# Kernel optimization log

Hardware: AMD Instinct MI355X
Metric: run time of the kernel (lower is better)

Reference implementation:

```python
import jax, jax.numpy as jnp
import numpy as np
import math

B, T, E, H = 2, 2048, 1024, 16
HD = E // H


def layernorm(x, g, b, eps=1e-5):
    mu = jnp.mean(x, axis=-1, keepdims=True)
    var = jnp.var(x, axis=-1, keepdims=True)
    return (x - mu) * jax.lax.rsqrt(var + eps) * g + b


def new_gelu(x):
    c = math.sqrt(2.0 / math.pi)
    return 0.5 * x * (1.0 + jnp.tanh(c * (x + 0.044715 * x ** 3)))


def setup_inputs() -> dict:
    key = jax.random.key(0)
    ks = jax.random.split(key, 6)
    s = 0.02
    return {
        "x": jax.random.normal(ks[0], (B, T, E), jnp.float32),
        "ln1_g": jnp.ones((E,), jnp.float32),
        "ln1_b": jnp.zeros((E,), jnp.float32),
        "w_attn": jax.random.normal(ks[1], (E, 3 * E), jnp.float32) * s,
        "b_attn": jnp.zeros((3 * E,), jnp.float32),
        "w_proj": jax.random.normal(ks[2], (E, E), jnp.float32) * s,
        "b_proj": jnp.zeros((E,), jnp.float32),
        "ln2_g": jnp.ones((E,), jnp.float32),
        "ln2_b": jnp.zeros((E,), jnp.float32),
        "w_fc": jax.random.normal(ks[3], (E, 4 * E), jnp.float32) * s,
        "b_fc": jnp.zeros((4 * E,), jnp.float32),
        "w_fc2": jax.random.normal(ks[4], (4 * E, E), jnp.float32) * s,
        "b_fc2": jnp.zeros((E,), jnp.float32),
    }


def reference(x, ln1_g, ln1_b, w_attn, b_attn, w_proj, b_proj,
              ln2_g, ln2_b, w_fc, b_fc, w_fc2, b_fc2):
    # --- attention branch (pre-norm) ---
    h = layernorm(x, ln1_g, ln1_b)
    qkv = h @ w_attn + b_attn                      # [B,T,3E]
    q, k, v = jnp.split(qkv, 3, axis=-1)
    # [B,T,E] -> [B,H,T,HD]
    q = q.reshape(B, T, H, HD).transpose(0, 2, 1, 3)
    k = k.reshape(B, T, H, HD).transpose(0, 2, 1, 3)
    v = v.reshape(B, T, H, HD).transpose(0, 2, 1, 3)
    att = jnp.einsum('bhqd,bhkd->bhqk', q, k) * (1.0 / math.sqrt(HD))
    causal = jnp.tril(jnp.ones((T, T), bool))       # [T,T]
    att = jnp.where(causal, att, -jnp.inf)
    att = jax.nn.softmax(att, axis=-1)
    y = jnp.einsum('bhqk,bhkd->bhqd', att, v)       # [B,H,T,HD]
    y = y.transpose(0, 2, 1, 3).reshape(B, T, E)
    y = y @ w_proj + b_proj
    x = x + y
    # --- MLP branch (pre-norm) ---
    h = layernorm(x, ln2_g, ln2_b)
    h = new_gelu(h @ w_fc + b_fc)
    h = h @ w_fc2 + b_fc2
    return x + h
```

## Files before the change

### kernel.cpp

```cpp
#include <hip/hip_runtime.h>

typedef unsigned short u16;
typedef unsigned int   u32;
typedef short bf16x8 __attribute__((ext_vector_type(8)));
typedef float f32x4  __attribute__((ext_vector_type(4)));

__device__ __forceinline__ float bf_lo(u32 u){ return __uint_as_float(u << 16); }
__device__ __forceinline__ float bf_hi(u32 u){ return __uint_as_float(u & 0xffff0000u); }
__device__ __forceinline__ u16 bf16r(float f){
  u32 u = __float_as_uint(f);
  u += 0x7fffu + ((u >> 16) & 1u);
  return (u16)(u >> 16);
}
__device__ __forceinline__ u32 pack2(float a, float b){
  return (u32)bf16r(a) | ((u32)bf16r(b) << 16);
}
__device__ __forceinline__ u32 pk_trunc(float a, float b){
  return (__float_as_uint(a) >> 16) | (__float_as_uint(b) & 0xffff0000u);
}
__device__ __forceinline__ float gelu_f(float x){
  float t = 0.7978845608028654f * (x + 0.044715f * x * x * x);
  t = fminf(fmaxf(t, -12.f), 12.f);
  float e = __expf(2.f * t);
  float th = (e - 1.f) / (e + 1.f);
  return 0.5f * x * (1.f + th);
}
__device__ __forceinline__ void glds16(const void* g, void* l) {
  __builtin_amdgcn_global_load_lds(
      (const __attribute__((address_space(1))) void*)g,
      (__attribute__((address_space(3))) void*)l, 16, 0, 0);
}

#define QSCALE 0.1803368801111204f

__global__ __launch_bounds__(256) void wt_k(const float* __restrict__ W,
                                            u16* __restrict__ Wt, int K, int N) {
  __shared__ float t[32][33];
  int k0 = blockIdx.x * 32, n0 = blockIdx.y * 32;
  int tx = threadIdx.x & 31, ty = threadIdx.x >> 5;
  #pragma unroll
  for (int i = 0; i < 32; i += 8)
    t[ty + i][tx] = W[(size_t)(k0 + ty + i) * N + n0 + tx];
  __syncthreads();
  #pragma unroll
  for (int i = 0; i < 32; i += 8)
    Wt[(size_t)(n0 + ty + i) * K + k0 + tx] = bf16r(t[tx][ty + i]);
}

__global__ __launch_bounds__(256) void vt_k(const u16* __restrict__ qkv,
                                            u16* __restrict__ Vt) {
  __shared__ u16 tl[32][33];
  int t0 = blockIdx.x * 32;
  int bh = blockIdx.y >> 1, d0 = (blockIdx.y & 1) * 32;
  int bb = bh >> 4, h = bh & 15;
  int tx = threadIdx.x & 31, ty = threadIdx.x >> 5;
  #pragma unroll
  for (int i = 0; i < 32; i += 8)
    tl[ty + i][tx] = qkv[(size_t)(bb*2048 + t0 + ty + i)*3072 + 2048 + h*64 + d0 + tx];
  __syncthreads();
  #pragma unroll
  for (int i = 0; i < 32; i += 8)
    Vt[((size_t)bh*64 + d0 + ty + i)*2048 + t0 + tx] = tl[tx][ty + i];
}

__global__ __launch_bounds__(256) void ln_k(const float* __restrict__ x,
                                            const float* __restrict__ g,
                                            const float* __restrict__ bta,
                                            u16* __restrict__ out) {
  int row = blockIdx.x, tid = threadIdx.x;
  const float4 xv = ((const float4*)(x + (size_t)row * 1024))[tid];
  float s = xv.x + xv.y + xv.z + xv.w;
  float q = xv.x*xv.x + xv.y*xv.y + xv.z*xv.z + xv.w*xv.w;
  #pragma unroll
  for (int off = 32; off > 0; off >>= 1) {
    s += __shfl_down(s, off);
    q += __shfl_down(q, off);
  }
  __shared__ float ss[4], sq[4];
  if ((tid & 63) == 0) { ss[tid >> 6] = s; sq[tid >> 6] = q; }
  __syncthreads();
  s = ss[0] + ss[1] + ss[2] + ss[3];
  q = sq[0] + sq[1] + sq[2] + sq[3];
  float mu = s * (1.f/1024.f);
  float rs = rsqrtf(q * (1.f/1024.f) - mu*mu + 1e-5f);
  const float4 gv = ((const float4*)g)[tid];
  const float4 bv = ((const float4*)bta)[tid];
  uint2 o;
  o.x = pack2((xv.x-mu)*rs*gv.x + bv.x, (xv.y-mu)*rs*gv.y + bv.y);
  o.y = pack2((xv.z-mu)*rs*gv.z + bv.z, (xv.w-mu)*rs*gv.w + bv.w);
  ((uint2*)(out + (size_t)row * 1024))[tid] = o;
}

template<int MODE, int MI, int LB>
__global__ __launch_bounds__(256, LB) void gemm_k(
    const u16* __restrict__ A, const u16* __restrict__ Bt,
    const float* __restrict__ bias, const float* __restrict__ resid,
    void* __restrict__ out, int M, int N, int K, int lda)
{
  constexpr int TM = MI * 32;
  __shared__ u16 Al[TM * 64];
  __shared__ u16 Bl[128 * 64];
  const int tid = threadIdx.x;
  const int by = blockIdx.y;
  const int sp = (MODE == 5) ? (by >> 3) : 0;
  const int n0 = (MODE == 5) ? ((by & 7) * 128) : (by * 128);
  const size_t koff = (size_t)sp * K;
  const int m0 = blockIdx.x * TM;
  const int wave = tid >> 6, lane = tid & 63;
  const int wm = (wave >> 1) * (MI * 16), wn = (wave & 1) * 64;
  const int l15 = lane & 15, quad = lane >> 4;
  const int sr = lane >> 3, cs = lane & 7;
  f32x4 acc[MI][4];
  const f32x4 zero = {0.f, 0.f, 0.f, 0.f};
  #pragma unroll
  for (int i = 0; i < MI; ++i)
    #pragma unroll
    for (int j = 0; j < 4; ++j)
      acc[i][j] = zero;
  for (int k0 = 0; k0 < K; k0 += 64) {
    __syncthreads();
    #pragma unroll
    for (int it = 0; it < MI; ++it) {
      int r = it*32 + wave*8 + sr;
      int c = cs ^ (r & 7);
      glds16(&A[(size_t)(m0 + r) * lda + koff + k0 + c*8], &Al[(it*32 + wave*8) * 64]);
    }
    #pragma unroll
    for (int it = 0; it < 4; ++it) {
      int r = it*32 + wave*8 + sr;
      int c = cs ^ (r & 7);
      glds16(&Bt[(size_t)(n0 + r) * lda + koff + k0 + c*8], &Bl[(it*32 + wave*8) * 64]);
    }
    __syncthreads();
    #pragma unroll
    for (int kk = 0; kk < 2; ++kk) {
      bf16x8 af[MI], bfr[4];
      #pragma unroll
      for (int i = 0; i < MI; ++i) {
        int R = wm + i*16 + l15;
        af[i] = *(const bf16x8*)&Al[R*64 + ((kk*4 + quad) ^ (R & 7)) * 8];
      }
      #pragma unroll
      for (int j = 0; j < 4; ++j) {
        int R = wn + j*16 + l15;
        bfr[j] = *(const bf16x8*)&Bl[R*64 + ((kk*4 + quad) ^ (R & 7)) * 8];
      }
      #pragma unroll
      for (int i = 0; i < MI; ++i)
        #pragma unroll
        for (int j = 0; j < 4; ++j)
          acc[i][j] = __builtin_amdgcn_mfma_f32_16x16x32_bf16(af[i], bfr[j], acc[i][j], 0, 0, 0);
    }
  }
  #pragma unroll
  for (int i = 0; i < MI; ++i) {
    #pragma unroll
    for (int j = 0; j < 4; ++j) {
      int col = n0 + wn + j*16 + l15;
      float bv = (MODE == 5) ? 0.f : bias[col];
      float sc = (MODE == 4 && col < 1024) ? QSCALE : 1.0f;
      #pragma unroll
      for (int r = 0; r < 4; ++r) {
        int row = m0 + wm + i*16 + quad*4 + r;
        size_t idx = (size_t)row * N + col;
        float v = acc[i][j][r] + bv;
        if constexpr (MODE == 0)      ((u16*)out)[idx] = bf16r(v);
        else if constexpr (MODE == 1) ((float*)out)[idx] = v + resid[idx];
        else if constexpr (MODE == 2) ((u16*)out)[idx] = bf16r(gelu_f(v));
        else if constexpr (MODE == 4) ((u16*)out)[idx] = bf16r(v * sc);
        else if constexpr (MODE == 5) ((u16*)out)[(size_t)sp*M*N + idx] = bf16r(v);
        else                          ((float*)out)[idx] = v + resid[idx];
      }
    }
  }
}

__global__ __launch_bounds__(256) void cmb_k(const u16* __restrict__ p,
                                             const float* __restrict__ bias,
                                             const float* __restrict__ x2,
                                             float* __restrict__ out) {
  int row = blockIdx.x, t = threadIdx.x;
  size_t i = (size_t)row * 1024 + t*4;
  uint2 a = *(const uint2*)&p[i];
  uint2 b = *(const uint2*)&p[4194304 + i];
  float4 xv = ((const float4*)x2)[i >> 2];
  float4 bv = ((const float4*)bias)[t];
  float4 o;
  o.x = bf_lo(a.x) + bf_lo(b.x) + bv.x + xv.x;
  o.y = bf_hi(a.x) + bf_hi(b.x) + bv.y + xv.y;
  o.z = bf_lo(a.y) + bf_lo(b.y) + bv.z + xv.z;
  o.w = bf_hi(a.y) + bf_hi(b.y) + bv.w + xv.w;
  ((float4*)out)[i >> 2] = o;
}

__global__ __launch_bounds__(256, 4) void attn_k(const u16* __restrict__ qkv,
                                                 const u16* __restrict__ Vt,
                                                 u16* __restrict__ y) {
  __shared__ u16 Kl[64*64];
  __shared__ u16 Vl[64*64];
  __shared__ u16 Pw[4*16*72];
  const int tid = threadIdx.x;
  const int bh = blockIdx.x & 31, bb = bh >> 4, h = bh & 15;
  const int qt = 31 - (int)(blockIdx.x >> 5);
  const int w = tid >> 6, lane = tid & 63;
  const int l15 = lane & 15, quad = lane >> 4;
  const int sr = lane >> 3, cs = lane & 7;
  u16* Pme = Pw + w * (16*72);
  const int w16l = w*16 + l15;
  const int dquad = quad*4;

  const u16* qp = qkv + ((size_t)(bb*2048 + qt*64 + w16l))*3072 + h*64 + quad*8;
  const bf16x8 aq0 = *(const bf16x8*)qp;
  const bf16x8 aq1 = *(const bf16x8*)(qp + 32);

  f32x4 o[4];
  const f32x4 zero = {0.f,0.f,0.f,0.f};
  #pragma unroll
  for (int dt = 0; dt < 4; ++dt) o[dt] = zero;
  float l = 0.f;

  const u16* kbase = qkv + (size_t)bb*2048*3072 + 1024 + h*64;
  const u16* vbase = Vt + (size_t)bh*64*2048;

  for (int kt = 0; kt <= qt; ++kt) {
    __syncthreads();
    #pragma unroll
    for (int it = 0; it < 2; ++it) {
      int r = it*32 + w*8 + sr;
      int c = cs ^ (r & 7);
      glds16(kbase + (size_t)(kt*64 + r)*3072 + c*8, &Kl[(it*32 + w*8) * 64]);
      glds16(vbase + (size_t)r*2048 + kt*64 + c*8,   &Vl[(it*32 + w*8) * 64]);
    }
    __syncthreads();
    bf16x8 ak[4][2], av[4][2];
    #pragma unroll
    for (int nt = 0; nt < 4; ++nt) {
      int R = nt*16 + l15;
      #pragma unroll
      for (int kk = 0; kk < 2; ++kk) {
        ak[nt][kk] = *(const bf16x8*)&Kl[R*64 + ((kk*4 + quad) ^ (R & 7)) * 8];
        av[nt][kk] = *(const bf16x8*)&Vl[R*64 + ((kk*4 + quad) ^ (R & 7)) * 8];
      }
    }
    f32x4 sv[4];
    #pragma unroll
    for (int nt = 0; nt < 4; ++nt) {
      f32x4 s = zero;
      s = __builtin_amdgcn_mfma_f32_16x16x32_bf16(ak[nt][0], aq0, s, 0, 0, 0);
      s = __builtin_amdgcn_mfma_f32_16x16x32_bf16(ak[nt][1], aq1, s, 0, 0, 0);
      sv[nt] = s;
    }
    if (kt == qt) {
      #pragma unroll
      for (int nt = 0; nt < 4; ++nt)
        #pragma unroll
        for (int r = 0; r < 4; ++r)
          if (nt*16 + dquad + r > w16l) sv[nt][r] = -1e30f;
    }
    float pv[4][4];
    #pragma unroll
    for (int nt = 0; nt < 4; ++nt)
      #pragma unroll
      for (int r = 0; r < 4; ++r)
        pv[nt][r] = exp2f(sv[nt][r]);
    l += ((pv[0][0]+pv[0][1])+(pv[0][2]+pv[0][3]))
       + ((pv[1][0]+pv[1][1])+(pv[1][2]+pv[1][3]))
       + ((pv[2][0]+pv[2][1])+(pv[2][2]+pv[2][3]))
       + ((pv[3][0]+pv[3][1])+(pv[3][2]+pv[3][3]));
    #pragma unroll
    for (int nt = 0; nt < 4; ++nt) {
      uint2 pr;
      pr.x = pk_trunc(pv[nt][0], pv[nt][1]);
      pr.y = pk_trunc(pv[nt][2], pv[nt][3]);
      *(uint2*)&Pme[l15*72 + nt*16 + dquad] = pr;
    }
    const bf16x8 bp0 = *(const bf16x8*)&Pme[l15*72 + quad*8];
    const bf16x8 bp1 = *(const bf16x8*)&Pme[l15*72 + 32 + quad*8];
    #pragma unroll
    for (int dt = 0; dt < 4; ++dt) {
      o[dt] = __builtin_amdgcn_mfma_f32_16x16x32_bf16(av[dt][0], bp0, o[dt], 0, 0, 0);
      o[dt] = __builtin_amdgcn_mfma_f32_16x16x32_bf16(av[dt][1], bp1, o[dt], 0, 0, 0);
    }
  }
  float lt = l;
  lt += __shfl_xor(lt, 16);
  lt += __shfl_xor(lt, 32);
  float inv = 1.f / lt;
  u16* yp = y + ((size_t)(bb*2048 + qt*64 + w16l))*1024 + h*64;
  #pragma unroll
  for (int dt = 0; dt < 4; ++dt) {
    uint2 pk;
    pk.x = pack2(o[dt][0]*inv, o[dt][1]*inv);
    pk.y = pack2(o[dt][2]*inv, o[dt][3]*inv);
    *(uint2*)(yp + dt*16 + dquad) = pk;
  }
}

extern "C" void kernel_launch(void* const* d_in, const int* in_sizes, int n_in,
                              void* d_out, int out_size, void* d_ws, size_t ws_size,
                              hipStream_t stream) {
  const float* x      = (const float*)d_in[0];
  const float* ln1_g  = (const float*)d_in[1];
  const float* ln1_b  = (const float*)d_in[2];
  const float* w_attn = (const float*)d_in[3];
  const float* b_attn = (const float*)d_in[4];
  const float* w_proj = (const float*)d_in[5];
  const float* b_proj = (const float*)d_in[6];
  const float* ln2_g  = (const float*)d_in[7];
  const float* ln2_b  = (const float*)d_in[8];
  const float* w_fc   = (const float*)d_in[9];
  const float* b_fc   = (const float*)d_in[10];
  const float* w_fc2  = (const float*)d_in[11];
  const float* b_fc2  = (const float*)d_in[12];

  char* ws = (char*)d_ws;
  u16*   wt_attn = (u16*)(ws);
  u16*   wt_proj = (u16*)(ws + 6291456);
  u16*   wt_fc   = (u16*)(ws + 8388608);
  u16*   wt_fc2  = (u16*)(ws + 16777216);
  u16*   h1      = (u16*)(ws + 25165824);
  u16*   qkvb    = (u16*)(ws + 33554432);
  u16*   yb      = (u16*)(ws + 58720256);
  float* x2      = (float*)(ws + 67108864);
  u16*   h2  = h1;
  u16*   vtb = h1;
  u16*   act = qkvb;
  u16*   pk2 = (u16*)(ws);

  wt_k<<<dim3(32, 96),  256, 0, stream>>>(w_attn, wt_attn, 1024, 3072);
  wt_k<<<dim3(32, 32),  256, 0, stream>>>(w_proj, wt_proj, 1024, 1024);
  wt_k<<<dim3(32, 128), 256, 0, stream>>>(w_fc,   wt_fc,   1024, 4096);
  wt_k<<<dim3(128, 32), 256, 0, stream>>>(w_fc2,  wt_fc2,  4096, 1024);

  ln_k<<<4096, 256, 0, stream>>>(x, ln1_g, ln1_b, h1);
  gemm_k<4,2,3><<<dim3(64, 24), 256, 0, stream>>>(h1, wt_attn, b_attn, nullptr,
                                                  (void*)qkvb, 4096, 3072, 1024, 1024);
  vt_k<<<dim3(64, 64), 256, 0, stream>>>(qkvb, vtb);
  attn_k<<<dim3(1024), 256, 0, stream>>>(qkvb, vtb, yb);
  gemm_k<1,2,3><<<dim3(64, 8), 256, 0, stream>>>(yb, wt_proj, b_proj, x,
                                                 (void*)x2, 4096, 1024, 1024, 1024);
  ln_k<<<4096, 256, 0, stream>>>(x2, ln2_g, ln2_b, h2);
  gemm_k<2,2,3><<<dim3(64, 32), 256, 0, stream>>>(h2, wt_fc, b_fc, nullptr,
                                                  (void*)act, 4096, 4096, 1024, 1024);
  gemm_k<5,2,3><<<dim3(64, 16), 256, 0, stream>>>(act, wt_fc2, b_fc2, nullptr,
                                                  (void*)pk2, 4096, 1024, 2048, 4096);
  cmb_k<<<4096, 256, 0, stream>>>(pk2, b_fc2, x2, (float*)d_out);
}
```

Before: 346.9 us.

## Fuse weight transposes with first layernorm and enlarge M tile for QKV/FC GEMMs

Merges the four weight-transpose launches and the first layernorm into one prep kernel that dispatches on block index, removing four kernel launches and the gaps between them. It also doubles the M tile (MI 2→4) for the QKV and FC1 GEMMs, halving the grid in M so each B tile loaded into shared memory is reused across more rows. The larger tile raises register and LDS use per block, which may lower occupancy under the unchanged launch bound of 3. With 32x24 = 768 blocks for QKV, the grid may also fill the device less evenly.

Measured after the change: 318.4 us. -8.2%, faster.

```diff
diff --git a/kernel.cpp b/kernel.cpp
--- a/kernel.cpp
+++ b/kernel.cpp
@@ -33,10 +33,11 @@
 
 #define QSCALE 0.1803368801111204f
 
-__global__ __launch_bounds__(256) void wt_k(const float* __restrict__ W,
-                                            u16* __restrict__ Wt, int K, int N) {
+__device__ __forceinline__ void wt_body(const float* __restrict__ W,
+                                        u16* __restrict__ Wt, int K, int N,
+                                        int kx, int nx) {
   __shared__ float t[32][33];
-  int k0 = blockIdx.x * 32, n0 = blockIdx.y * 32;
+  int k0 = kx * 32, n0 = nx * 32;
   int tx = threadIdx.x & 31, ty = threadIdx.x >> 5;
   #pragma unroll
   for (int i = 0; i < 32; i += 8)
@@ -47,27 +48,11 @@
     Wt[(size_t)(n0 + ty + i) * K + k0 + tx] = bf16r(t[tx][ty + i]);
 }
 
-__global__ __launch_bounds__(256) void vt_k(const u16* __restrict__ qkv,
-                                            u16* __restrict__ Vt) {
-  __shared__ u16 tl[32][33];
-  int t0 = blockIdx.x * 32;
-  int bh = blockIdx.y >> 1, d0 = (blockIdx.y & 1) * 32;
-  int bb = bh >> 4, h = bh & 15;
-  int tx = threadIdx.x & 31, ty = threadIdx.x >> 5;
-  #pragma unroll
-  for (int i = 0; i < 32; i += 8)
-    tl[ty + i][tx] = qkv[(size_t)(bb*2048 + t0 + ty + i)*3072 + 2048 + h*64 + d0 + tx];
-  __syncthreads();
-  #pragma unroll
-  for (int i = 0; i < 32; i += 8)
-    Vt[((size_t)bh*64 + d0 + ty + i)*2048 + t0 + tx] = tl[tx][ty + i];
-}
-
-__global__ __launch_bounds__(256) void ln_k(const float* __restrict__ x,
-                                            const float* __restrict__ g,
-                                            const float* __restrict__ bta,
-                                            u16* __restrict__ out) {
-  int row = blockIdx.x, tid = threadIdx.x;
+__device__ __forceinline__ void ln_body(const float* __restrict__ x,
+                                        const float* __restrict__ g,
+                                        const float* __restrict__ bta,
+                                        u16* __restrict__ out, int row) {
+  int tid = threadIdx.x;
   const float4 xv = ((const float4*)(x + (size_t)row * 1024))[tid];
   float s = xv.x + xv.y + xv.z + xv.w;
   float q = xv.x*xv.x + xv.y*xv.y + xv.z*xv.z + xv.w*xv.w;
@@ -89,6 +74,45 @@
   o.x = pack2((xv.x-mu)*rs*gv.x + bv.x, (xv.y-mu)*rs*gv.y + bv.y);
   o.y = pack2((xv.z-mu)*rs*gv.z + bv.z, (xv.w-mu)*rs*gv.w + bv.w);
   ((uint2*)(out + (size_t)row * 1024))[tid] = o;
+}
+
+__global__ __launch_bounds__(256) void prep_k(
+    const float* __restrict__ w_attn, const float* __restrict__ w_proj,
+    const float* __restrict__ w_fc,   const float* __restrict__ w_fc2,
+    u16* __restrict__ wt_attn, u16* __restrict__ wt_proj,
+    u16* __restrict__ wt_fc,   u16* __restrict__ wt_fc2,
+    const float* __restrict__ x, const float* __restrict__ g,
+    const float* __restrict__ b, u16* __restrict__ h1)
+{
+  int i = blockIdx.x;
+  if (i < 3072)       wt_body(w_attn, wt_attn, 1024, 3072, i & 31, i >> 5);
+  else if (i < 4096)  { int j = i - 3072; wt_body(w_proj, wt_proj, 1024, 1024, j & 31, j >> 5); }
+  else if (i < 8192)  { int j = i - 4096; wt_body(w_fc,   wt_fc,   1024, 4096, j & 31, j >> 5); }
+  else if (i < 12288) { int j = i - 8192; wt_body(w_fc2,  wt_fc2,  4096, 1024, j & 127, j >> 7); }
+  else                ln_body(x, g, b, h1, i - 12288);
+}
+
+__global__ __launch_bounds__(256) void vt_k(const u16* __restrict__ qkv,
+                                            u16* __restrict__ Vt) {
+  __shared__ u16 tl[32][33];
+  int t0 = blockIdx.x * 32;
+  int bh = blockIdx.y >> 1, d0 = (blockIdx.y & 1) * 32;
+  int bb = bh >> 4, h = bh & 15;
+  int tx = threadIdx.x & 31, ty = threadIdx.x >> 5;
+  #pragma unroll
+  for (int i = 0; i < 32; i += 8)
+    tl[ty + i][tx] = qkv[(size_t)(bb*2048 + t0 + ty + i)*3072 + 2048 + h*64 + d0 + tx];
+  __syncthreads();
+  #pragma unroll
+  for (int i = 0; i < 32; i += 8)
+    Vt[((size_t)bh*64 + d0 + ty + i)*2048 + t0 + tx] = tl[tx][ty + i];
+}
+
+__global__ __launch_bounds__(256) void ln_k(const float* __restrict__ x,
+                                            const float* __restrict__ g,
+                                            const float* __restrict__ bta,
+                                            u16* __restrict__ out) {
+  ln_body(x, g, bta, out, blockIdx.x);
 }
 
 template<int MODE, int MI, int LB>
@@ -327,20 +351,17 @@
   u16*   act = qkvb;
   u16*   pk2 = (u16*)(ws);
 
-  wt_k<<<dim3(32, 96),  256, 0, stream>>>(w_attn, wt_attn, 1024, 3072);
-  wt_k<<<dim3(32, 32),  256, 0, stream>>>(w_proj, wt_proj, 1024, 1024);
-  wt_k<<<dim3(32, 128), 256, 0, stream>>>(w_fc,   wt_fc,   1024, 4096);
-  wt_k<<<dim3(128, 32), 256, 0, stream>>>(w_fc2,  wt_fc2,  4096, 1024);
-
-  ln_k<<<4096, 256, 0, stream>>>(x, ln1_g, ln1_b, h1);
-  gemm_k<4,2,3><<<dim3(64, 24), 256, 0, stream>>>(h1, wt_attn, b_attn, nullptr,
+  prep_k<<<dim3(16384), 256, 0, stream>>>(w_attn, w_proj, w_fc, w_fc2,
+                                          wt_attn, wt_proj, wt_fc, wt_fc2,
+                                          x, ln1_g, ln1_b, h1);
+  gemm_k<4,4,3><<<dim3(32, 24), 256, 0, stream>>>(h1, wt_attn, b_attn, nullptr,
                                                   (void*)qkvb, 4096, 3072, 1024, 1024);
   vt_k<<<dim3(64, 64), 256, 0, stream>>>(qkvb, vtb);
   attn_k<<<dim3(1024), 256, 0, stream>>>(qkvb, vtb, yb);
   gemm_k<1,2,3><<<dim3(64, 8), 256, 0, stream>>>(yb, wt_proj, b_proj, x,
                                                  (void*)x2, 4096, 1024, 1024, 1024);
   ln_k<<<4096, 256, 0, stream>>>(x2, ln2_g, ln2_b, h2);
-  gemm_k<2,2,3><<<dim3(64, 32), 256, 0, stream>>>(h2, wt_fc, b_fc, nullptr,
+  gemm_k<2,4,3><<<dim3(32, 32), 256, 0, stream>>>(h2, wt_fc, b_fc, nullptr,
                                                   (void*)act, 4096, 4096, 1024, 1024);
   gemm_k<5,2,3><<<dim3(64, 16), 256, 0, stream>>>(act, wt_fc2, b_fc2, nullptr,
                                                   (void*)pk2, 4096, 1024, 2048, 4096);
```
